# Optimization experiments

Hardware: AMD Instinct MI355X
Metric: run time of the kernel (lower is better)

## Reference

```python
import jax, jax.numpy as jnp
import numpy as np

CD_WEIGHT = 100.0


def setup_inputs() -> dict:
    key = jax.random.key(0)
    k1, k2 = jax.random.split(key)
    array1 = jax.random.normal(k1, (4, 4096, 3), dtype=jnp.float32)
    array2 = jax.random.normal(k2, (4, 4096, 3), dtype=jnp.float32)
    return {"array1": array1, "array2": array2}


def _chamfer(a1, a2):
    # a1: [B, N, D], a2: [B, M, D]
    # squared pairwise distances d2[b, n, m] = ||a1[b,n] - a2[b,m]||^2
    # computed as ||a||^2 + ||b||^2 - 2 a.b to avoid materializing [B,N,M,D]
    sq1 = jnp.sum(a1 * a1, axis=-1)                      # [B, N]
    sq2 = jnp.sum(a2 * a2, axis=-1)                      # [B, M]
    cross = jnp.einsum("bnd,bmd->bnm", a1, a2)           # [B, N, M]
    d2 = sq1[:, :, None] + sq2[:, None, :] - 2.0 * cross  # [B, N, M]
    # av_dist1: for each array2 point, min over array1 points, then mean
    av_dist1 = jnp.mean(jnp.min(d2, axis=1), axis=-1)    # [B]
    # av_dist2: for each array1 point, min over array2 points, then mean
    av_dist2 = jnp.mean(jnp.min(d2, axis=2), axis=-1)    # [B]
    return CD_WEIGHT * jnp.mean(0.5 * (av_dist1 + av_dist2))


def reference(array1, array2):
    return _chamfer(array1, array2)
```

## Files before the change

kernel.cpp:

```cpp
#include <hip/hip_runtime.h>
#include <math.h>


#define NPTS   4096
#define NBATCH 4
#define RSPLIT 4
#define RCHUNK (NPTS / RSPLIT)
#define QPB    256
#define SCALE  (50.0f / (float)(NBATCH * NPTS))

__global__ __launch_bounds__(QPB) void chamfer_stage1(
    const float* __restrict__ a1, const float* __restrict__ a2,
    float* __restrict__ pm)
{
    __shared__ float4 refs[RCHUNK];

    const int b    = blockIdx.y;
    const int dir  = blockIdx.z >> 2;
    const int h    = blockIdx.z & 3;
    const float* q = (dir == 0) ? a1 : a2;
    const float* r = (dir == 0) ? a2 : a1;
    q += (size_t)b * NPTS * 3;
    r += (size_t)b * NPTS * 3;

    const int base = h * RCHUNK;
    for (int j = threadIdx.x; j < RCHUNK; j += QPB) {
        const int g = base + j;
        float rx = r[3 * g + 0];
        float ry = r[3 * g + 1];
        float rz = r[3 * g + 2];
        float r2 = rx * rx + ry * ry + rz * rz;
        refs[j] = make_float4(rx, ry, rz, r2);
    }
    __syncthreads();

    const int qi = blockIdx.x * QPB + threadIdx.x;
    const float qx = q[3 * qi + 0];
    const float qy = q[3 * qi + 1];
    const float qz = q[3 * qi + 2];
    const float q2  = qx * qx + qy * qy + qz * qz;
    const float qx2 = -2.0f * qx;
    const float qy2 = -2.0f * qy;
    const float qz2 = -2.0f * qz;

    float m0 = INFINITY, m1 = INFINITY, m2 = INFINITY, m3 = INFINITY;
    #pragma unroll 4
    for (int j = 0; j < RCHUNK; j += 4) {
        float4 p0 = refs[j + 0];
        float4 p1 = refs[j + 1];
        float4 p2 = refs[j + 2];
        float4 p3 = refs[j + 3];
        float t0 = fmaf(qz2, p0.z, fmaf(qy2, p0.y, fmaf(qx2, p0.x, p0.w)));
        float t1 = fmaf(qz2, p1.z, fmaf(qy2, p1.y, fmaf(qx2, p1.x, p1.w)));
        float t2 = fmaf(qz2, p2.z, fmaf(qy2, p2.y, fmaf(qx2, p2.x, p2.w)));
        float t3 = fmaf(qz2, p3.z, fmaf(qy2, p3.y, fmaf(qx2, p3.x, p3.w)));
        m0 = fminf(m0, t0);
        m1 = fminf(m1, t1);
        m2 = fminf(m2, t2);
        m3 = fminf(m3, t3);
    }
    float m = fminf(fminf(m0, m1), fminf(m2, m3)) + q2;

    const int qg = ((dir * NBATCH + b) * NPTS + qi);
    pm[qg * RSPLIT + h] = m;
}

__global__ __launch_bounds__(1024) void chamfer_stage2(
    const float4* __restrict__ pm, float* __restrict__ out)
{
    __shared__ float wsum[16];
    const int nq = 2 * NBATCH * NPTS;
    float s = 0.0f;
    for (int qg = threadIdx.x; qg < nq; qg += 1024) {
        float4 p = pm[qg];
        s += fminf(fminf(p.x, p.y), fminf(p.z, p.w));
    }
    for (int off = 32; off > 0; off >>= 1) s += __shfl_down(s, off);
    if ((threadIdx.x & 63) == 0) wsum[threadIdx.x >> 6] = s;
    __syncthreads();
    if (threadIdx.x < 64) {
        float v = (threadIdx.x < 16) ? wsum[threadIdx.x] : 0.0f;
        for (int off = 8; off > 0; off >>= 1) v += __shfl_down(v, off);
        if (threadIdx.x == 0) out[0] = v * SCALE;
    }
}

extern "C" void kernel_launch(void* const* d_in, const int* in_sizes, int n_in,
                              void* d_out, int out_size, void* d_ws, size_t ws_size,
                              hipStream_t stream) {
    const float* a1 = (const float*)d_in[0];
    const float* a2 = (const float*)d_in[1];
    float* out = (float*)d_out;
    float* pm  = (float*)d_ws;

    chamfer_stage1<<<dim3(NPTS / QPB, NBATCH, 2 * RSPLIT), QPB, 0, stream>>>(a1, a2, pm);
    chamfer_stage2<<<1, 1024, 0, stream>>>((const float4*)pm, out);
}
```

Before: 85.91 us.

## Register-block eight queries per thread and split reduction across blocks

Each thread now handles eight query points, so every reference point read from shared memory is reused across eight distance computations, which cuts LDS traffic per FMA. The reference set is split into 32 chunks instead of 4 to keep enough blocks in flight, and partial minima are stored chunk-major. The final reduction becomes a multi-block min-and-sum kernel followed by a tiny sum kernel, replacing the single-block reduction. The cost is more partial-min memory traffic and an extra launch.

```diff
diff --git a/kernel.cpp b/kernel.cpp
--- a/kernel.cpp
+++ b/kernel.cpp
@@ -2,12 +2,15 @@
 #include <math.h>
 
 
-#define NPTS   4096
-#define NBATCH 4
-#define RSPLIT 4
-#define RCHUNK (NPTS / RSPLIT)
-#define QPB    256
-#define SCALE  (50.0f / (float)(NBATCH * NPTS))
+#define NPTS     4096
+#define NBATCH   4
+#define RSPLIT   32
+#define RCHUNK   (NPTS / RSPLIT)
+#define QPB      256
+#define QPT      8
+#define QBLK     (QPB * QPT)
+#define NQTOT    (2 * NBATCH * NPTS)
+#define SCALE    (50.0f / (float)(NBATCH * NPTS))
 
 __global__ __launch_bounds__(QPB) void chamfer_stage1(
     const float* __restrict__ a1, const float* __restrict__ a2,
@@ -15,74 +18,84 @@
 {
     __shared__ float4 refs[RCHUNK];
 
-    const int b    = blockIdx.y;
-    const int dir  = blockIdx.z >> 2;
-    const int h    = blockIdx.z & 3;
+    const int b   = blockIdx.y;
+    const int dir = blockIdx.z >> 5;
+    const int c   = blockIdx.z & 31;
     const float* q = (dir == 0) ? a1 : a2;
     const float* r = (dir == 0) ? a2 : a1;
     q += (size_t)b * NPTS * 3;
     r += (size_t)b * NPTS * 3;
 
-    const int base = h * RCHUNK;
-    for (int j = threadIdx.x; j < RCHUNK; j += QPB) {
-        const int g = base + j;
+    if (threadIdx.x < RCHUNK) {
+        const int g = c * RCHUNK + threadIdx.x;
         float rx = r[3 * g + 0];
         float ry = r[3 * g + 1];
         float rz = r[3 * g + 2];
-        float r2 = rx * rx + ry * ry + rz * rz;
-        refs[j] = make_float4(rx, ry, rz, r2);
+        refs[threadIdx.x] = make_float4(rx, ry, rz, rx * rx + ry * ry + rz * rz);
+    }
+
+    const int q0 = blockIdx.x * QBLK + threadIdx.x;
+    float qx2[QPT], qy2[QPT], qz2[QPT], q2[QPT];
+    #pragma unroll
+    for (int k = 0; k < QPT; ++k) {
+        const int qi = q0 + k * QPB;
+        float x = q[3 * qi + 0];
+        float y = q[3 * qi + 1];
+        float z = q[3 * qi + 2];
+        q2[k]  = x * x + y * y + z * z;
+        qx2[k] = -2.0f * x;
+        qy2[k] = -2.0f * y;
+        qz2[k] = -2.0f * z;
     }
     __syncthreads();
 
-    const int qi = blockIdx.x * QPB + threadIdx.x;
-    const float qx = q[3 * qi + 0];
-    const float qy = q[3 * qi + 1];
-    const float qz = q[3 * qi + 2];
-    const float q2  = qx * qx + qy * qy + qz * qz;
-    const float qx2 = -2.0f * qx;
-    const float qy2 = -2.0f * qy;
-    const float qz2 = -2.0f * qz;
+    float mins[QPT];
+    #pragma unroll
+    for (int k = 0; k < QPT; ++k) mins[k] = INFINITY;
 
-    float m0 = INFINITY, m1 = INFINITY, m2 = INFINITY, m3 = INFINITY;
-    #pragma unroll 4
-    for (int j = 0; j < RCHUNK; j += 4) {
-        float4 p0 = refs[j + 0];
-        float4 p1 = refs[j + 1];
-        float4 p2 = refs[j + 2];
-        float4 p3 = refs[j + 3];
-        float t0 = fmaf(qz2, p0.z, fmaf(qy2, p0.y, fmaf(qx2, p0.x, p0.w)));
-        float t1 = fmaf(qz2, p1.z, fmaf(qy2, p1.y, fmaf(qx2, p1.x, p1.w)));
-        float t2 = fmaf(qz2, p2.z, fmaf(qy2, p2.y, fmaf(qx2, p2.x, p2.w)));
-        float t3 = fmaf(qz2, p3.z, fmaf(qy2, p3.y, fmaf(qx2, p3.x, p3.w)));
-        m0 = fminf(m0, t0);
-        m1 = fminf(m1, t1);
-        m2 = fminf(m2, t2);
-        m3 = fminf(m3, t3);
+    #pragma unroll 2
+    for (int j = 0; j < RCHUNK; ++j) {
+        float4 p = refs[j];
+        #pragma unroll
+        for (int k = 0; k < QPT; ++k) {
+            float t = fmaf(qz2[k], p.z,
+                      fmaf(qy2[k], p.y,
+                      fmaf(qx2[k], p.x, p.w)));
+            mins[k] = fminf(mins[k], t);
+        }
     }
-    float m = fminf(fminf(m0, m1), fminf(m2, m3)) + q2;
 
-    const int qg = ((dir * NBATCH + b) * NPTS + qi);
-    pm[qg * RSPLIT + h] = m;
+    const int qgbase = (dir * NBATCH + b) * NPTS + q0;
+    #pragma unroll
+    for (int k = 0; k < QPT; ++k) {
+        pm[(size_t)c * NQTOT + qgbase + k * QPB] = mins[k] + q2[k];
+    }
 }
 
-__global__ __launch_bounds__(1024) void chamfer_stage2(
-    const float4* __restrict__ pm, float* __restrict__ out)
+__global__ __launch_bounds__(256) void chamfer_stage2(
+    const float* __restrict__ pm, float* __restrict__ psum)
 {
-    __shared__ float wsum[16];
-    const int nq = 2 * NBATCH * NPTS;
-    float s = 0.0f;
-    for (int qg = threadIdx.x; qg < nq; qg += 1024) {
-        float4 p = pm[qg];
-        s += fminf(fminf(p.x, p.y), fminf(p.z, p.w));
-    }
+    const int qg = blockIdx.x * 256 + threadIdx.x;
+    float m = INFINITY;
+    #pragma unroll
+    for (int c = 0; c < RSPLIT; ++c)
+        m = fminf(m, pm[(size_t)c * NQTOT + qg]);
+
+    float s = m;
     for (int off = 32; off > 0; off >>= 1) s += __shfl_down(s, off);
+    __shared__ float wsum[4];
     if ((threadIdx.x & 63) == 0) wsum[threadIdx.x >> 6] = s;
     __syncthreads();
-    if (threadIdx.x < 64) {
-        float v = (threadIdx.x < 16) ? wsum[threadIdx.x] : 0.0f;
-        for (int off = 8; off > 0; off >>= 1) v += __shfl_down(v, off);
-        if (threadIdx.x == 0) out[0] = v * SCALE;
-    }
+    if (threadIdx.x == 0)
+        psum[blockIdx.x] = wsum[0] + wsum[1] + wsum[2] + wsum[3];
+}
+
+__global__ __launch_bounds__(64) void chamfer_stage3(
+    const float* __restrict__ psum, float* __restrict__ out)
+{
+    float s = psum[threadIdx.x] + psum[threadIdx.x + 64];
+    for (int off = 32; off > 0; off >>= 1) s += __shfl_down(s, off);
+    if (threadIdx.x == 0) out[0] = s * SCALE;
 }
 
 extern "C" void kernel_launch(void* const* d_in, const int* in_sizes, int n_in,
@@ -90,9 +103,11 @@
                               hipStream_t stream) {
     const float* a1 = (const float*)d_in[0];
     const float* a2 = (const float*)d_in[1];
-    float* out = (float*)d_out;
-    float* pm  = (float*)d_ws;
+    float* out  = (float*)d_out;
+    float* pm   = (float*)d_ws;
+    float* psum = (float*)((char*)d_ws + (size_t)RSPLIT * NQTOT * sizeof(float));
 
-    chamfer_stage1<<<dim3(NPTS / QPB, NBATCH, 2 * RSPLIT), QPB, 0, stream>>>(a1, a2, pm);
-    chamfer_stage2<<<1, 1024, 0, stream>>>((const float4*)pm, out);
+    chamfer_stage1<<<dim3(NPTS / QBLK, NBATCH, 2 * RSPLIT), QPB, 0, stream>>>(a1, a2, pm);
+    chamfer_stage2<<<NQTOT / 256, 256, 0, stream>>>(pm, psum);
+    chamfer_stage3<<<1, 64, 0, stream>>>(psum, out);
 }
```

Result: faster. 72.31 us (-15.8%).
